# Kernel optimization log

Measured on AMD Instinct MI355X. Metric: run time of the kernel, lower is better.

Reference implementation:

```python
import jax, jax.numpy as jnp
import numpy as np

N_NODES = 10000
N_EDGES = 320000
AVG_NEIGH = 32.0


def ssp(x):
    # ShiftedSoftPlus
    return jax.nn.softplus(x) - jnp.asarray(np.log(2.0), x.dtype)


def setup_inputs() -> dict:
    key = jax.random.key(0)
    ks = jax.random.split(key, 16)
    inp = {
        "node_feats0": jax.random.normal(ks[0], (N_NODES, 64), jnp.float32),
        "node_feats1": jax.random.normal(ks[1], (N_NODES, 64, 3), jnp.float32),
        "node_attrs": jax.random.uniform(ks[2], (N_NODES, 4), jnp.float32),
        "edge_embedding": jax.random.uniform(ks[3], (N_EDGES, 8), jnp.float32),
        "edge_attrs": jax.random.normal(ks[4], (N_EDGES, 4), jnp.float32),
        "edge_src": jax.random.randint(ks[5], (N_EDGES,), 0, N_NODES),
        "edge_dst": jax.random.randint(ks[6], (N_EDGES,), 0, N_NODES),
        "W1_0": jax.random.normal(ks[7], (64, 64), jnp.float32),
        "W1_1": jax.random.normal(ks[8], (64, 64), jnp.float32),
        "Wr1": jax.random.normal(ks[9], (8, 8), jnp.float32),
        "Wr2": jax.random.normal(ks[10], (8, 256), jnp.float32),
        "W2_0": jax.random.normal(ks[11], (128, 128), jnp.float32),
        "W2_1": jax.random.normal(ks[12], (128, 64), jnp.float32),
        "Wsc_0": jax.random.normal(ks[13], (64, 4, 128), jnp.float32),
        "Wsc_1": jax.random.normal(ks[14], (64, 4, 64), jnp.float32),
    }
    return inp


def _tfn_layer(node_feats0, node_feats1, node_attrs, edge_embedding, edge_attrs,
               edge_src, edge_dst, W1_0, W1_1, Wr1, Wr2, W2_0, W2_1, Wsc_0, Wsc_1):
    N = node_feats0.shape[0]
    # --- linear_1 (e3nn Linear: per-irrep block, 1/sqrt(fan_in)) ---
    x0 = (node_feats0 @ W1_0) / jnp.sqrt(64.0)                       # [N,64]
    x1 = jnp.einsum('nuc,uw->nwc', node_feats1, W1_1) / jnp.sqrt(64.0)  # [N,64,3]
    # --- radial MLP: 8 -> 8 (ssp) -> 256, no bias ---
    h = ssp(edge_embedding @ Wr1 / jnp.sqrt(8.0))
    w = (h @ Wr2 / jnp.sqrt(8.0)).reshape(-1, 4, 64)                  # [E,4,64]
    # --- gather source node features ---
    xs0 = x0[edge_src]                                                # [E,64]
    xs1 = x1[edge_src]                                                # [E,64,3]
    y0 = edge_attrs[:, 0:1]                                           # [E,1] (0e SH)
    y1 = edge_attrs[:, 1:4]                                           # [E,3] (1o SH)
    # --- per-edge equivariant tensor product (uvu, 4 instructions) ---
    m00 = w[:, 0] * xs0 * y0                                          # 0e x 0e -> 0e
    m01 = w[:, 1][:, :, None] * xs0[:, :, None] * y1[:, None, :]      # 0e x 1o -> 1o
    m10 = w[:, 2][:, :, None] * xs1 * y0[:, :, None]                  # 1o x 0e -> 1o
    m11 = w[:, 3] * jnp.einsum('euc,ec->eu', xs1, y1) / jnp.sqrt(3.0)  # 1o x 1o -> 0e
    mid0 = jnp.concatenate([m00, m11], axis=1)                        # [E,128]
    mid1 = jnp.concatenate([m01, m10], axis=1)                        # [E,128,3]
    # --- scatter-sum to destination nodes, / sqrt(avg_num_neighbors) ---
    agg0 = jax.ops.segment_sum(mid0, edge_dst, num_segments=N) / jnp.sqrt(AVG_NEIGH)
    agg1 = jax.ops.segment_sum(mid1, edge_dst, num_segments=N) / jnp.sqrt(AVG_NEIGH)
    # --- linear_2 to conv output irreps 128x0e + 64x1o ---
    out0 = (agg0 @ W2_0) / jnp.sqrt(128.0)                            # [N,128]
    out1 = jnp.einsum('nuc,uw->nwc', agg1, W2_1) / jnp.sqrt(128.0)    # [N,64,3]
    # --- self connection: FullyConnectedTensorProduct(node_feats_in, node_attrs) ---
    sc0 = jnp.einsum('nu,nv,uvw->nw', node_feats0, node_attrs, Wsc_0) / jnp.sqrt(256.0)
    sc1 = jnp.einsum('nuc,nv,uvw->nwc', node_feats1, node_attrs, Wsc_1) / jnp.sqrt(256.0)
    n0 = out0 + sc0
    n1 = out1 + sc1
    # --- Gate nonlinearity: 64 scalars (ssp), 64 gates (ssp) gating 64x1o ---
    scalars = ssp(n0[:, :64])
    gates = ssp(n0[:, 64:])
    gated = n1 * gates[:, :, None]
    # --- resnet ---
    new0 = node_feats0 + scalars
    new1 = node_feats1 + gated
    return jnp.concatenate([new0, new1.reshape(N, 192)], axis=1)      # [N,256]


def reference(node_feats0, node_feats1, node_attrs, edge_embedding, edge_attrs,
              edge_src, edge_dst, W1_0, W1_1, Wr1, Wr2, W2_0, W2_1, Wsc_0, Wsc_1):
    return _tfn_layer(node_feats0, node_feats1, node_attrs, edge_embedding, edge_attrs,
                      edge_src, edge_dst, W1_0, W1_1, Wr1, Wr2, W2_0, W2_1, Wsc_0, Wsc_1)
```

## Files before the change

kernel.cpp:

```cpp
#include <hip/hip_runtime.h>
#include <math.h>

#define N_NODES 10000
#define N_EDGES 320000
#define DEG_CAP 96

typedef short bf16x8 __attribute__((ext_vector_type(8)));
typedef float f32x4 __attribute__((ext_vector_type(4)));

__device__ __forceinline__ float ssp(float x) {
    float ax = fabsf(x);
    return fmaxf(x, 0.0f) + log1pf(expf(-ax)) - 0.69314718055994531f;
}
__device__ __forceinline__ float bcastf(float v, int l) {
    return __uint_as_float(__builtin_amdgcn_readlane(__float_as_uint(v), l));
}
__device__ __forceinline__ int bcasti(int v, int l) {
    return __builtin_amdgcn_readlane(v, l);
}
__device__ __forceinline__ int div3(int q) {
    return (q * 21846) >> 16;
}
__device__ __forceinline__ unsigned short f2bf(float f) {
    unsigned int u = __float_as_uint(f);
    u += 0x7fff + ((u >> 16) & 1);
    return (unsigned short)(u >> 16);
}


__global__ __launch_bounds__(256) void wprep_kernel(
    const float* __restrict__ W2_0, const float* __restrict__ Wsc0,
    const float* __restrict__ W2_1, const float* __restrict__ Wsc1,
    uint4* __restrict__ wb0, uint4* __restrict__ wb1)
{
    const int tid = blockIdx.x*256 + threadIdx.x;
    const float rs128 = 0.088388347648318447f;
    const float s16 = 0.0625f;
    if (tid < 6144) {
        const int kstep = tid >> 9;
        const int rem = tid & 511;
        const int col = ((rem >> 6) << 4) + (rem & 15);
        const int kb = kstep*32 + (((rem & 63) >> 4) << 3);
        unsigned int u[4];
        #pragma unroll
        for (int h = 0; h < 4; ++h) {
            const int k0 = kb + 2*h, k1 = k0 + 1;
            const float f0 = (k0 < 128) ? W2_0[k0*128+col]*rs128 : Wsc0[(k0-128)*128+col]*s16;
            const float f1 = (k1 < 128) ? W2_0[k1*128+col]*rs128 : Wsc0[(k1-128)*128+col]*s16;
            u[h] = (unsigned int)f2bf(f0) | ((unsigned int)f2bf(f1) << 16);
        }
        wb0[tid] = make_uint4(u[0], u[1], u[2], u[3]);
    } else if (tid < 9216) {
        const int t2 = tid - 6144;
        const int kstep = t2 >> 8;
        const int rem = t2 & 255;
        const int col = ((rem >> 6) << 4) + (rem & 15);
        const int kb = kstep*32 + (((rem & 63) >> 4) << 3);
        unsigned int u[4];
        #pragma unroll
        for (int h = 0; h < 4; ++h) {
            const int k0 = kb + 2*h, k1 = k0 + 1;
            const float f0 = (k0 < 128) ? W2_1[k0*64+col]*rs128 : Wsc1[(k0-128)*64+col]*s16;
            const float f1 = (k1 < 128) ? W2_1[k1*64+col]*rs128 : Wsc1[(k1-128)*64+col]*s16;
            u[h] = (unsigned int)f2bf(f0) | ((unsigned int)f2bf(f1) << 16);
        }
        wb1[t2] = make_uint4(u[0], u[1], u[2], u[3]);
    }
}


__global__ __launch_bounds__(256) void node_pre_kernel(
        const float* __restrict__ nf0, const float* __restrict__ nf1,
        const float* __restrict__ W1_0, const float* __restrict__ W1_1,
        const int* __restrict__ edst, const int* __restrict__ esrc,
        int* __restrict__ counts, int2* __restrict__ csr2,
        uint2* __restrict__ xpack) {
    const int n = blockIdx.x;
    const int t = threadIdx.x;
    __shared__ float s_f0[64];
    __shared__ float s_f1[192];
    __shared__ unsigned short sx[4][64];
    if (t < 64) s_f0[t] = nf0[n*64 + t];
    else        s_f1[t-64] = nf1[n*192 + (t-64)];
    if (t >= 224) {
        int e = n*32 + (t - 224);
        int d = edst[e];
        int sv = esrc[e];
        int p = atomicAdd(&counts[d], 1);
        if (p < DEG_CAP) csr2[d * DEG_CAP + p] = make_int2(e, sv);
    }
    __syncthreads();
    if (t < 64) {
        float acc = 0.f;
        #pragma unroll 8
        for (int u = 0; u < 64; ++u) acc += s_f0[u] * W1_0[u*64 + t];
        sx[0][t] = f2bf(acc * 0.125f);
    } else {
        const int c = (t - 64) >> 6;
        const int w = t & 63;
        float acc = 0.f;
        #pragma unroll 8
        for (int u = 0; u < 64; ++u) acc += s_f1[u*3 + c] * W1_1[u*64 + w];
        sx[1+c][w] = f2bf(acc * 0.125f);
    }
    __syncthreads();
    if (t < 64) {
        uint2 v;
        v.x = (unsigned int)sx[0][t] | ((unsigned int)sx[1][t] << 16);
        v.y = (unsigned int)sx[2][t] | ((unsigned int)sx[3][t] << 16);
        xpack[(size_t)n*64 + t] = v;
    }
}


__global__ __launch_bounds__(64, 4) void edge_kernel(
    const float* __restrict__ eemb, const float* __restrict__ eattr,
    const int* __restrict__ counts, const int2* __restrict__ csr2,
    const uint2* __restrict__ xpack,
    const float* __restrict__ Wr1, const float* __restrict__ Wr2,
    unsigned int* __restrict__ agg0p, unsigned int* __restrict__ agg1p)
{
    const int n = blockIdx.x;
    const int u = threadIdx.x;
    const int j8 = u & 7;

    const float rs8 = 0.35355339059327373f;
    const float rs3 = 0.57735026918962576f;

    float wr2[4][8];
    #pragma unroll
    for (int k = 0; k < 4; ++k) {
        #pragma unroll
        for (int j = 0; j < 8; ++j) {
            float v = Wr2[j*256 + k*64 + u] * rs8;
            wr2[k][j] = (k == 3) ? v * rs3 : v;
        }
    }
    float wr1c[8];
    #pragma unroll
    for (int i = 0; i < 8; ++i) wr1c[i] = Wr1[i*8 + j8] * rs8;

    float A[8] = {0.f,0.f,0.f,0.f,0.f,0.f,0.f,0.f};

    const int craw = counts[n];
    const int cnt  = craw < DEG_CAP ? craw : DEG_CAP;
    const int base0 = n * DEG_CAP;

    int2 es = make_int2(0, 0);
    float4 m0 = {0,0,0,0}, m1 = {0,0,0,0};
    float yy = 0.f;
    uint2 g[8];
    #pragma unroll
    for (int s = 0; s < 8; ++s) g[s] = make_uint2(0u, 0u);

    if (0 < cnt) {
        const int mm = cnt < 8 ? cnt : 8;
        const int sl = (u >> 3) < mm ? (u >> 3) : 0;
        es = csr2[base0 + sl];
        m0 = *reinterpret_cast<const float4*>(eemb + (size_t)es.x*8);
        m1 = *reinterpret_cast<const float4*>(eemb + (size_t)es.x*8 + 4);
        yy = eattr[(size_t)es.x*4 + (j8 & 3)];
        #pragma unroll
        for (int s = 0; s < 8; ++s)
            g[s] = xpack[(size_t)bcasti(es.y, s*8)*64 + u];
    }

    for (int b = 0; b < cnt; b += 8) {
        const int m = cnt - b < 8 ? cnt - b : 8;
        const float4 cm0 = m0, cm1 = m1;
        const float cy = yy;
        uint2 cg[8];
        #pragma unroll
        for (int s = 0; s < 8; ++s) cg[s] = g[s];

        const int bn = b + 8;
        const bool more = (bn < cnt);
        int2 esn = make_int2(0, 0);
        if (more) {
            const int mn = cnt - bn < 8 ? cnt - bn : 8;
            const int sn = (u >> 3) < mn ? (u >> 3) : 0;
            esn = csr2[base0 + bn + sn];
        }

        float pre = cm0.x*wr1c[0] + cm0.y*wr1c[1] + cm0.z*wr1c[2] + cm0.w*wr1c[3]
                  + cm1.x*wr1c[4] + cm1.y*wr1c[5] + cm1.z*wr1c[6] + cm1.w*wr1c[7];
        const float h = ssp(pre);

        if (more) {
            es = esn;
            m0 = *reinterpret_cast<const float4*>(eemb + (size_t)es.x*8);
            m1 = *reinterpret_cast<const float4*>(eemb + (size_t)es.x*8 + 4);
            yy = eattr[(size_t)es.x*4 + (j8 & 3)];
            #pragma unroll
            for (int s = 0; s < 8; ++s)
                g[s] = xpack[(size_t)bcasti(es.y, s*8)*64 + u];
        }

        #pragma unroll
        for (int s = 0; s < 8; ++s) {
            if (s >= m) break;
            const int bs = s * 8;
            const float xs0 = __uint_as_float(cg[s].x << 16);
            const float x1a = __uint_as_float(cg[s].x & 0xffff0000u);
            const float x1b = __uint_as_float(cg[s].y << 16);
            const float x1c = __uint_as_float(cg[s].y & 0xffff0000u);
            float w0 = 0.f, w1 = 0.f, w2 = 0.f, w3 = 0.f;
            #pragma unroll
            for (int j = 0; j < 8; ++j) {
                const float hj = bcastf(h, bs + j);
                w0 += hj * wr2[0][j];
                w1 += hj * wr2[1][j];
                w2 += hj * wr2[2][j];
                w3 += hj * wr2[3][j];
            }
            const float y0 = bcastf(cy, bs+0);
            const float y1 = bcastf(cy, bs+1);
            const float y2 = bcastf(cy, bs+2);
            const float y3 = bcastf(cy, bs+3);
            A[0] += w0 * xs0 * y0;
            const float t01 = w1 * xs0;
            A[1] += t01*y1; A[2] += t01*y2; A[3] += t01*y3;
            const float t10 = w2 * y0;
            A[4] += t10*x1a; A[5] += t10*x1b; A[6] += t10*x1c;
            A[7] += w3 * (x1a*y1 + x1b*y2 + x1c*y3);
        }
    }

    const float rs32 = 0.17677669529663687f;
    float v[8], pv[8];
    #pragma unroll
    for (int a = 0; a < 8; ++a) {
        v[a] = A[a] * rs32;
        pv[a] = __shfl_xor(v[a], 1);
    }
    if (!(u & 1)) {
        const int kp = u >> 1;
        unsigned int pk[8];
        #pragma unroll
        for (int a = 0; a < 8; ++a)
            pk[a] = (unsigned int)f2bf(v[a]) | ((unsigned int)f2bf(pv[a]) << 16);
        agg0p[(size_t)n*64 + kp]      = pk[0];
        agg0p[(size_t)n*64 + 32 + kp] = pk[7];
        #pragma unroll
        for (int c = 0; c < 3; ++c) {
            agg1p[(size_t)n*192 + c*64 + kp]      = pk[1+c];
            agg1p[(size_t)n*192 + c*64 + 32 + kp] = pk[4+c];
        }
    }
}


__global__ __launch_bounds__(512) void epiA_mfma_kernel(
    const float* __restrict__ nf0, const float* __restrict__ nattr,
    const unsigned int* __restrict__ agg0p, const uint4* __restrict__ wb0,
    float* __restrict__ out, float* __restrict__ gbuf)
{
    __shared__ unsigned int sA[3072];
    const int t = threadIdx.x;
    const int node0 = blockIdx.x * 16;

    #pragma unroll
    for (int it = 0; it < 6; ++it) {
        int idx = it*512 + t;
        int q = idx >> 6;
        int row = div3(q);
        int seg = q - 3*row;
        int kp = seg*64 + (idx & 63);
        int node = node0 + row;
        unsigned int val;
        if (kp < 64) val = agg0p[(size_t)node*64 + kp];
        else {
            int pk = kp - 64;
            float f = nf0[(size_t)node*64 + (pk >> 1)];
            const float2 at = *reinterpret_cast<const float2*>(nattr + (size_t)node*4 + ((pk & 1) << 1));
            val = (unsigned int)f2bf(f*at.x) | ((unsigned int)f2bf(f*at.y) << 16);
        }
        sA[row*192 + (kp ^ ((row & 7) << 2))] = val;
    }
    __syncthreads();

    const int ct = t >> 6;
    const int lane = t & 63;
    const int m = lane & 15;
    const int ks = lane >> 4;
    const char* sab = reinterpret_cast<const char*>(sA) + m*768;
    const int swz = (m & 7) << 4;

    f32x4 acc = {0.f, 0.f, 0.f, 0.f};
    #pragma unroll
    for (int kstep = 0; kstep < 12; ++kstep) {
        bf16x8 a = *reinterpret_cast<const bf16x8*>(sab + (((kstep << 6) + (ks << 4)) ^ swz));
        bf16x8 b = *reinterpret_cast<const bf16x8*>(wb0 + (kstep << 9) + (ct << 6) + lane);
        acc = __builtin_amdgcn_mfma_f32_16x16x32_bf16(a, b, acc, 0, 0, 0);
    }

    const int col = ct*16 + m;
    #pragma unroll
    for (int q = 0; q < 4; ++q) {
        const int node = node0 + ks*4 + q;
        const float v = ssp(acc[q]);
        if (col < 64) out[(size_t)node*256 + col] = nf0[(size_t)node*64 + col] + v;
        else          gbuf[(size_t)node*64 + (col - 64)] = v;
    }
}


__global__ __launch_bounds__(256) void epiB_mfma_kernel(
    const float* __restrict__ nf1, const float* __restrict__ nattr,
    const unsigned int* __restrict__ agg1p, const uint4* __restrict__ wb1,
    const float* __restrict__ gbuf, float* __restrict__ out)
{
    __shared__ unsigned int sB[3072];
    const int t = threadIdx.x;
    const int row0 = blockIdx.x * 16;

    #pragma unroll
    for (int it = 0; it < 12; ++it) {
        int idx = it*256 + t;
        int q = idx >> 6;
        int row = div3(q);
        int seg = q - 3*row;
        int kp = seg*64 + (idx & 63);
        int r = row0 + row;
        int n = div3(r);
        int c = r - 3*n;
        unsigned int val;
        if (kp < 64) val = agg1p[(size_t)n*192 + c*64 + kp];
        else {
            int pk = kp - 64;
            float f = nf1[(size_t)n*192 + (pk >> 1)*3 + c];
            const float2 at = *reinterpret_cast<const float2*>(nattr + (size_t)n*4 + ((pk & 1) << 1));
            val = (unsigned int)f2bf(f*at.x) | ((unsigned int)f2bf(f*at.y) << 16);
        }
        sB[row*192 + (kp ^ ((row & 7) << 2))] = val;
    }
    __syncthreads();

    const int ct = t >> 6;
    const int lane = t & 63;
    const int m = lane & 15;
    const int ks = lane >> 4;
    const char* sab = reinterpret_cast<const char*>(sB) + m*768;
    const int swz = (m & 7) << 4;

    f32x4 acc = {0.f, 0.f, 0.f, 0.f};
    #pragma unroll
    for (int kstep = 0; kstep < 12; ++kstep) {
        bf16x8 a = *reinterpret_cast<const bf16x8*>(sab + (((kstep << 6) + (ks << 4)) ^ swz));
        bf16x8 b = *reinterpret_cast<const bf16x8*>(wb1 + (kstep << 8) + (ct << 6) + lane);
        acc = __builtin_amdgcn_mfma_f32_16x16x32_bf16(a, b, acc, 0, 0, 0);
    }

    const int col = ct*16 + m;
    #pragma unroll
    for (int q = 0; q < 4; ++q) {
        const int r = row0 + ks*4 + q;
        const int n = div3(r);
        const int c = r - 3*n;
        const float g = gbuf[(size_t)n*64 + col];
        out[(size_t)n*256 + 64 + col*3 + c] = nf1[(size_t)n*192 + col*3 + c] + acc[q]*g;
    }
}


extern "C" void kernel_launch(void* const* d_in, const int* in_sizes, int n_in,
                              void* d_out, int out_size, void* d_ws, size_t ws_size,
                              hipStream_t stream) {
    const float* nf0   = (const float*)d_in[0];
    const float* nf1   = (const float*)d_in[1];
    const float* nattr = (const float*)d_in[2];
    const float* eemb  = (const float*)d_in[3];
    const float* eattr = (const float*)d_in[4];
    const int*   esrc  = (const int*)d_in[5];
    const int*   edst  = (const int*)d_in[6];
    const float* W1_0  = (const float*)d_in[7];
    const float* W1_1  = (const float*)d_in[8];
    const float* Wr1   = (const float*)d_in[9];
    const float* Wr2   = (const float*)d_in[10];
    const float* W2_0  = (const float*)d_in[11];
    const float* W2_1  = (const float*)d_in[12];
    const float* Wsc0  = (const float*)d_in[13];
    const float* Wsc1  = (const float*)d_in[14];
    float* out = (float*)d_out;

    char* ws = (char*)d_ws;
    uint2* xpack = (uint2*)ws;         ws += (size_t)N_NODES*64*sizeof(uint2);
    int* counts  = (int*)ws;           ws += (size_t)N_NODES*sizeof(int);
    int2* csr2   = (int2*)ws;          ws += (size_t)N_NODES*DEG_CAP*sizeof(int2);
    unsigned int* agg0p = (unsigned int*)ws;
                                       ws += (size_t)N_NODES*64*sizeof(unsigned int);
    unsigned int* agg1p = (unsigned int*)ws;
                                       ws += (size_t)N_NODES*192*sizeof(unsigned int);
    uint4* wb0   = (uint4*)ws;         ws += (size_t)6144*sizeof(uint4);
    uint4* wb1   = (uint4*)ws;         ws += (size_t)3072*sizeof(uint4);
    float* gbuf  = (float*)csr2;

    hipMemsetAsync(counts, 0, N_NODES*sizeof(int), stream);
    wprep_kernel<<<36, 256, 0, stream>>>(W2_0, Wsc0, W2_1, Wsc1, wb0, wb1);
    node_pre_kernel<<<N_NODES, 256, 0, stream>>>(nf0, nf1, W1_0, W1_1, edst, esrc,
        counts, csr2, xpack);
    edge_kernel<<<N_NODES, 64, 0, stream>>>(eemb, eattr, counts, csr2,
        xpack, Wr1, Wr2, agg0p, agg1p);
    epiA_mfma_kernel<<<N_NODES/16, 512, 0, stream>>>(nf0, nattr, agg0p, wb0, out, gbuf);
    epiB_mfma_kernel<<<(3*N_NODES)/16, 256, 0, stream>>>(nf1, nattr, agg1p, wb1, gbuf, out);
}
```

Baseline: 125.8 us.

## Fold weight prep into node_pre, use fp16 dot2 for radial weights

Removes the separate wprep kernel launch by doing the bf16 weight packing in the first 36 blocks of node_pre_kernel. In the edge kernel the radial second-layer weights are packed into fp16 pairs and the per-edge weight contraction uses v_dot2 with packed hidden activations, halving the readlane broadcasts and FMAs. This also frees registers, and launch bounds are raised to 8 waves per EU to allow higher occupancy. The change trades precision for speed, since the radial weights and activations go through fp16 with round-toward-zero conversion.

```diff
diff --git a/kernel.cpp b/kernel.cpp
--- a/kernel.cpp
+++ b/kernel.cpp
@@ -7,6 +7,8 @@
 
 typedef short bf16x8 __attribute__((ext_vector_type(8)));
 typedef float f32x4 __attribute__((ext_vector_type(4)));
+typedef _Float16 f16x2 __attribute__((ext_vector_type(2)));
+typedef __fp16 fp16x2 __attribute__((ext_vector_type(2)));
 
 __device__ __forceinline__ float ssp(float x) {
     float ax = fabsf(x);
@@ -26,46 +28,13 @@
     u += 0x7fff + ((u >> 16) & 1);
     return (unsigned short)(u >> 16);
 }
-
-
-__global__ __launch_bounds__(256) void wprep_kernel(
-    const float* __restrict__ W2_0, const float* __restrict__ Wsc0,
-    const float* __restrict__ W2_1, const float* __restrict__ Wsc1,
-    uint4* __restrict__ wb0, uint4* __restrict__ wb1)
-{
-    const int tid = blockIdx.x*256 + threadIdx.x;
-    const float rs128 = 0.088388347648318447f;
-    const float s16 = 0.0625f;
-    if (tid < 6144) {
-        const int kstep = tid >> 9;
-        const int rem = tid & 511;
-        const int col = ((rem >> 6) << 4) + (rem & 15);
-        const int kb = kstep*32 + (((rem & 63) >> 4) << 3);
-        unsigned int u[4];
-        #pragma unroll
-        for (int h = 0; h < 4; ++h) {
-            const int k0 = kb + 2*h, k1 = k0 + 1;
-            const float f0 = (k0 < 128) ? W2_0[k0*128+col]*rs128 : Wsc0[(k0-128)*128+col]*s16;
-            const float f1 = (k1 < 128) ? W2_0[k1*128+col]*rs128 : Wsc0[(k1-128)*128+col]*s16;
-            u[h] = (unsigned int)f2bf(f0) | ((unsigned int)f2bf(f1) << 16);
-        }
-        wb0[tid] = make_uint4(u[0], u[1], u[2], u[3]);
-    } else if (tid < 9216) {
-        const int t2 = tid - 6144;
-        const int kstep = t2 >> 8;
-        const int rem = t2 & 255;
-        const int col = ((rem >> 6) << 4) + (rem & 15);
-        const int kb = kstep*32 + (((rem & 63) >> 4) << 3);
-        unsigned int u[4];
-        #pragma unroll
-        for (int h = 0; h < 4; ++h) {
-            const int k0 = kb + 2*h, k1 = k0 + 1;
-            const float f0 = (k0 < 128) ? W2_1[k0*64+col]*rs128 : Wsc1[(k0-128)*64+col]*s16;
-            const float f1 = (k1 < 128) ? W2_1[k1*64+col]*rs128 : Wsc1[(k1-128)*64+col]*s16;
-            u[h] = (unsigned int)f2bf(f0) | ((unsigned int)f2bf(f1) << 16);
-        }
-        wb1[t2] = make_uint4(u[0], u[1], u[2], u[3]);
-    }
+__device__ __forceinline__ unsigned int pkf16(float a, float b) {
+    union { fp16x2 v; unsigned int u; } cv;
+    cv.v = __builtin_amdgcn_cvt_pkrtz(a, b);
+    return cv.u;
+}
+__device__ __forceinline__ f16x2 u2h(unsigned int x) {
+    union { unsigned int u; f16x2 v; } cv; cv.u = x; return cv.v;
 }
 
 
@@ -74,7 +43,10 @@
         const float* __restrict__ W1_0, const float* __restrict__ W1_1,
         const int* __restrict__ edst, const int* __restrict__ esrc,
         int* __restrict__ counts, int2* __restrict__ csr2,
-        uint2* __restrict__ xpack) {
+        uint2* __restrict__ xpack,
+        const float* __restrict__ W2_0, const float* __restrict__ Wsc0,
+        const float* __restrict__ W2_1, const float* __restrict__ Wsc1,
+        uint4* __restrict__ wb0, uint4* __restrict__ wb1) {
     const int n = blockIdx.x;
     const int t = threadIdx.x;
     __shared__ float s_f0[64];
@@ -110,10 +82,43 @@
         v.y = (unsigned int)sx[2][t] | ((unsigned int)sx[3][t] << 16);
         xpack[(size_t)n*64 + t] = v;
     }
-}
-
-
-__global__ __launch_bounds__(64, 4) void edge_kernel(
+    const int tid = n*256 + t;
+    const float rs128 = 0.088388347648318447f;
+    const float s16 = 0.0625f;
+    if (tid < 6144) {
+        const int kstep = tid >> 9;
+        const int rem = tid & 511;
+        const int col = ((rem >> 6) << 4) + (rem & 15);
+        const int kb = kstep*32 + (((rem & 63) >> 4) << 3);
+        unsigned int u[4];
+        #pragma unroll
+        for (int h = 0; h < 4; ++h) {
+            const int k0 = kb + 2*h, k1 = k0 + 1;
+            const float f0 = (k0 < 128) ? W2_0[k0*128+col]*rs128 : Wsc0[(k0-128)*128+col]*s16;
+            const float f1 = (k1 < 128) ? W2_0[k1*128+col]*rs128 : Wsc0[(k1-128)*128+col]*s16;
+            u[h] = (unsigned int)f2bf(f0) | ((unsigned int)f2bf(f1) << 16);
+        }
+        wb0[tid] = make_uint4(u[0], u[1], u[2], u[3]);
+    } else if (tid < 9216) {
+        const int t2 = tid - 6144;
+        const int kstep = t2 >> 8;
+        const int rem = t2 & 255;
+        const int col = ((rem >> 6) << 4) + (rem & 15);
+        const int kb = kstep*32 + (((rem & 63) >> 4) << 3);
+        unsigned int u[4];
+        #pragma unroll
+        for (int h = 0; h < 4; ++h) {
+            const int k0 = kb + 2*h, k1 = k0 + 1;
+            const float f0 = (k0 < 128) ? W2_1[k0*64+col]*rs128 : Wsc1[(k0-128)*64+col]*s16;
+            const float f1 = (k1 < 128) ? W2_1[k1*64+col]*rs128 : Wsc1[(k1-128)*64+col]*s16;
+            u[h] = (unsigned int)f2bf(f0) | ((unsigned int)f2bf(f1) << 16);
+        }
+        wb1[t2] = make_uint4(u[0], u[1], u[2], u[3]);
+    }
+}
+
+
+__global__ __launch_bounds__(64, 8) void edge_kernel(
     const float* __restrict__ eemb, const float* __restrict__ eattr,
     const int* __restrict__ counts, const int2* __restrict__ csr2,
     const uint2* __restrict__ xpack,
@@ -127,13 +132,15 @@
     const float rs8 = 0.35355339059327373f;
     const float rs3 = 0.57735026918962576f;
 
-    float wr2[4][8];
+    unsigned int wr2p[4][4];
     #pragma unroll
     for (int k = 0; k < 4; ++k) {
         #pragma unroll
-        for (int j = 0; j < 8; ++j) {
-            float v = Wr2[j*256 + k*64 + u] * rs8;
-            wr2[k][j] = (k == 3) ? v * rs3 : v;
+        for (int jp = 0; jp < 4; ++jp) {
+            float a = Wr2[(2*jp)*256 + k*64 + u] * rs8;
+            float b = Wr2[(2*jp+1)*256 + k*64 + u] * rs8;
+            if (k == 3) { a *= rs3; b *= rs3; }
+            wr2p[k][jp] = pkf16(a, b);
         }
     }
     float wr1c[8];
@@ -185,6 +192,8 @@
         float pre = cm0.x*wr1c[0] + cm0.y*wr1c[1] + cm0.z*wr1c[2] + cm0.w*wr1c[3]
                   + cm1.x*wr1c[4] + cm1.y*wr1c[5] + cm1.z*wr1c[6] + cm1.w*wr1c[7];
         const float h = ssp(pre);
+        const float hn = __shfl_xor(h, 1);
+        const unsigned int hpu = (u & 1) ? pkf16(hn, h) : pkf16(h, hn);
 
         if (more) {
             es = esn;
@@ -206,12 +215,12 @@
             const float x1c = __uint_as_float(cg[s].y & 0xffff0000u);
             float w0 = 0.f, w1 = 0.f, w2 = 0.f, w3 = 0.f;
             #pragma unroll
-            for (int j = 0; j < 8; ++j) {
-                const float hj = bcastf(h, bs + j);
-                w0 += hj * wr2[0][j];
-                w1 += hj * wr2[1][j];
-                w2 += hj * wr2[2][j];
-                w3 += hj * wr2[3][j];
+            for (int jp = 0; jp < 4; ++jp) {
+                const f16x2 hj = u2h((unsigned int)bcasti((int)hpu, bs + 2*jp));
+                w0 = __builtin_amdgcn_fdot2(hj, u2h(wr2p[0][jp]), w0, false);
+                w1 = __builtin_amdgcn_fdot2(hj, u2h(wr2p[1][jp]), w1, false);
+                w2 = __builtin_amdgcn_fdot2(hj, u2h(wr2p[2][jp]), w2, false);
+                w3 = __builtin_amdgcn_fdot2(hj, u2h(wr2p[3][jp]), w3, false);
             }
             const float y0 = bcastf(cy, bs+0);
             const float y1 = bcastf(cy, bs+1);
@@ -396,9 +405,8 @@
     float* gbuf  = (float*)csr2;
 
     hipMemsetAsync(counts, 0, N_NODES*sizeof(int), stream);
-    wprep_kernel<<<36, 256, 0, stream>>>(W2_0, Wsc0, W2_1, Wsc1, wb0, wb1);
     node_pre_kernel<<<N_NODES, 256, 0, stream>>>(nf0, nf1, W1_0, W1_1, edst, esrc,
-        counts, csr2, xpack);
+        counts, csr2, xpack, W2_0, Wsc0, W2_1, Wsc1, wb0, wb1);
     edge_kernel<<<N_NODES, 64, 0, stream>>>(eemb, eattr, counts, csr2,
         xpack, Wr1, Wr2, agg0p, agg1p);
     epiA_mfma_kernel<<<N_NODES/16, 512, 0, stream>>>(nf0, nattr, agg0p, wb0, out, gbuf);
```

After: 217.5 us. 1.73x slower.
